# Optimization experiments

Measured on AMD Instinct MI355X. Metric: run time of the kernel, lower is better.

## Reference

```python
import jax, jax.numpy as jnp
import numpy as np

N = 50000      # nodes
D = 128        # in = hidden = out channels
L = 3          # num_layers
E = 320000     # edges per edge type
EPS_BN = 1e-5
EPS_NORM = 1e-12


def setup_inputs() -> dict:
    key = jax.random.key(0)
    ks = jax.random.split(key, 16)
    s = 1.0 / np.sqrt(D)
    inp = {}
    inp['x'] = jax.random.normal(ks[0], (N, D), jnp.float32)
    inp['edge_index0'] = jax.random.randint(ks[1], (2, E), 0, N, jnp.int32)
    inp['edge_index1'] = jax.random.randint(ks[2], (2, E), 0, N, jnp.int32)
    inp['W0'] = jax.random.normal(ks[3], (L, D, D), jnp.float32) * s
    inp['b0'] = jnp.zeros((L, D), jnp.float32)
    inp['W1'] = jax.random.normal(ks[4], (L, D, D), jnp.float32) * s
    inp['b1'] = jnp.zeros((L, D), jnp.float32)
    inp['gamma'] = jnp.ones((L, D), jnp.float32)
    inp['beta'] = jnp.zeros((L, D), jnp.float32)
    inp['emb1_W'] = jax.random.normal(ks[5], (D, D), jnp.float32) * s
    inp['emb1_b'] = jnp.zeros((D,), jnp.float32)
    inp['emb2_W'] = jax.random.normal(ks[6], (D, D), jnp.float32) * s
    inp['emb2_b'] = jnp.zeros((D,), jnp.float32)
    inp['ph1_Wa'] = jax.random.normal(ks[7], (D, D), jnp.float32) * s
    inp['ph1_ba'] = jnp.zeros((D,), jnp.float32)
    inp['ph1_Wb'] = jax.random.normal(ks[8], (D, D), jnp.float32) * s
    inp['ph1_bb'] = jnp.zeros((D,), jnp.float32)
    inp['ph2_Wa'] = jax.random.normal(ks[9], (D, D), jnp.float32) * s
    inp['ph2_ba'] = jnp.zeros((D,), jnp.float32)
    inp['ph2_Wb'] = jax.random.normal(ks[10], (D, D), jnp.float32) * s
    inp['ph2_bb'] = jnp.zeros((D,), jnp.float32)
    return inp


def _gcn(h_in, W, b, src, dst):
    # PyG GCNConv: add self-loops, symmetric deg^{-1/2} normalization, then scatter-add.
    h = h_in @ W                                   # [N, D]
    ones = jnp.ones(src.shape[0], h.dtype)
    deg = jax.ops.segment_sum(ones, dst, num_segments=N) + 1.0   # +1 self-loop
    dinv = jax.lax.rsqrt(deg)
    coef = (dinv[src] * dinv[dst])[:, None]        # [E, 1]
    agg = jax.ops.segment_sum(h[src] * coef, dst, num_segments=N)
    agg = agg + h * (dinv * dinv)[:, None]         # self-loop contribution
    return agg + b


def _bn(x, g, bt):
    # training-mode BatchNorm1d (batch statistics, biased variance)
    mu = jnp.mean(x, axis=0)
    var = jnp.mean(jnp.square(x - mu), axis=0)
    return (x - mu) * jax.lax.rsqrt(var + EPS_BN) * g + bt


def _l2norm(x):
    n = jnp.sqrt(jnp.sum(x * x, axis=1, keepdims=True))
    return x / jnp.maximum(n, EPS_NORM)


def reference(x, edge_index0, edge_index1, W0, b0, W1, b1, gamma, beta,
              emb1_W, emb1_b, emb2_W, emb2_b,
              ph1_Wa, ph1_ba, ph1_Wb, ph1_bb,
              ph2_Wa, ph2_ba, ph2_Wb, ph2_bb):
    s0, d0 = edge_index0[0], edge_index0[1]
    s1, d1 = edge_index1[0], edge_index1[1]
    h = x
    for i in range(L):
        # HeteroConv with aggr='sum': sum of the two edge-type GCNConv outputs
        h = _gcn(h, W0[i], b0[i], s0, d0) + _gcn(h, W1[i], b1[i], s1, d1)
        h = _bn(h, gamma[i], beta[i])
        if i < L - 1:
            h = jax.nn.relu(h)   # dropout omitted (deterministic / eval)
    e1 = jnp.tanh(h @ emb1_W + emb1_b)
    e2 = _l2norm(jnp.tanh(h @ emb2_W + emb2_b))
    p1 = _l2norm(jax.nn.relu(e1 @ ph1_Wa + ph1_ba) @ ph1_Wb + ph1_bb)
    p2 = _l2norm(jax.nn.relu(e2 @ ph2_Wa + ph2_ba) @ ph2_Wb + ph2_bb)
    return (e1, e2, p1, p2)
```

## Files before the change

### kernel.cpp

```cpp
#include <hip/hip_runtime.h>
#include <cstdint>
#include <cstddef>

#define D 128

typedef __attribute__((ext_vector_type(8))) short bf16x8;
typedef __attribute__((ext_vector_type(4))) float f32x4;
typedef __attribute__((ext_vector_type(8))) _Float16 f16x8;

__device__ __forceinline__ unsigned short f2bf(float f) {
  unsigned int u = __float_as_uint(f);
  unsigned int r = u + 0x7FFFu + ((u >> 16) & 1u);
  return (unsigned short)(r >> 16);
}
__device__ __forceinline__ float bf2f(unsigned short h) {
  return __uint_as_float((unsigned int)h << 16);
}
__device__ __forceinline__ float fast_tanh(float x) {
  float cx = fminf(fmaxf(x, -15.f), 15.f);
  float e = __expf(2.f * cx);
  return (e - 1.f) * __builtin_amdgcn_rcpf(e + 1.f);
}

struct WPtrs { const float* w[12]; };

__global__ __launch_bounds__(256) void packcount_kernel(
    WPtrs P, unsigned short* __restrict__ Wp,
    const int* __restrict__ d0, const int* __restrict__ d1,
    int* __restrict__ cnt, int E, int N, int packBlocks) {
  if ((int)blockIdx.x < packBlocks) {
    int tid = blockIdx.x * 256 + threadIdx.x;
    int m = tid >> 14;
    int r = tid & 16383;
    int b = r & 7, lane = (r >> 3) & 63, ks = (r >> 9) & 3, jt = r >> 11;
    int k = ks * 32 + ((lane >> 4) << 3) + b;
    int j = jt * 16 + (lane & 15);
    float w = P.w[m][k * 128 + j];
    unsigned short h = f2bf(w);
    Wp[m * 32768 + r] = h;
    Wp[m * 32768 + 16384 + r] = f2bf(w - bf2f(h));
  } else {
    int e = ((int)blockIdx.x - packBlocks) * 256 + threadIdx.x;
    if (e < E) {
      atomicAdd(&cnt[d0[e]], 1);
      atomicAdd(&cnt[N + d1[e]], 1);
    }
  }
}

__global__ __launch_bounds__(256) void scan_part_kernel(const int* __restrict__ cnt,
                                                        int* __restrict__ off,
                                                        int* __restrict__ bsum, int n2) {
  __shared__ int sh[256];
  int t = threadIdx.x;
  int i0 = blockIdx.x * 512 + 2 * t;
  int a0 = (i0 < n2) ? cnt[i0] : 0;
  int a1 = (i0 + 1 < n2) ? cnt[i0 + 1] : 0;
  int s = a0 + a1;
  sh[t] = s;
  __syncthreads();
  for (int d = 1; d < 256; d <<= 1) {
    int v = (t >= d) ? sh[t - d] : 0;
    __syncthreads();
    sh[t] += v;
    __syncthreads();
  }
  int p = sh[t] - s;
  if (i0 < n2) off[i0] = p;
  if (i0 + 1 < n2) off[i0 + 1] = p + a0;
  if (t == 255) bsum[blockIdx.x] = sh[255];
}

__global__ __launch_bounds__(256) void scan_bsum_kernel(int* __restrict__ bsum, int nb,
                                                        int* __restrict__ off_total) {
  __shared__ int sh[256];
  int t = threadIdx.x;
  int s = (t < nb) ? bsum[t] : 0;
  sh[t] = s;
  __syncthreads();
  for (int d = 1; d < 256; d <<= 1) {
    int v = (t >= d) ? sh[t - d] : 0;
    __syncthreads();
    sh[t] += v;
    __syncthreads();
  }
  if (t < nb) bsum[t] = sh[t] - s;
  if (t == 255) *off_total = sh[255];
}

__global__ __launch_bounds__(256) void scan_add_kernel(int* __restrict__ off,
                                                       const int* __restrict__ bsum,
                                                       int* __restrict__ cnt,
                                                       float* __restrict__ dinv, int n2) {
  int add = bsum[blockIdx.x];
  int base = blockIdx.x * 512;
#pragma unroll
  for (int u = 0; u < 2; u++) {
    int i = base + threadIdx.x + u * 256;
    if (i < n2) {
      off[i] += add;
      dinv[i] = rsqrtf((float)cnt[i] + 1.0f);
      cnt[i] = 0;
    }
  }
}

__global__ void fill_kernel(const int* __restrict__ ei0, const int* __restrict__ ei1,
                            const int* __restrict__ off, int* __restrict__ cnt,
                            int* __restrict__ csr, int E, int N) {
  int e = blockIdx.x * blockDim.x + threadIdx.x;
  if (e < E) {
    int s = ei0[e], d = ei0[E + e];
    int p = atomicAdd(&cnt[d], 1);
    csr[off[d] + p] = s;
    s = ei1[e]; d = ei1[E + e];
    p = atomicAdd(&cnt[N + d], 1);
    csr[off[N + d] + p] = s;
  }
}

__device__ __forceinline__ void split8(const float vv[8], bf16x8& hh, bf16x8& hl) {
#pragma unroll
  for (int c = 0; c < 8; c++) {
    unsigned short h = f2bf(vv[c]);
    hh[c] = (short)h;
    hl[c] = (short)f2bf(vv[c] - bf2f(h));
  }
}

template <int BN>
__global__ __launch_bounds__(256) void mm_dual(
    const unsigned short* __restrict__ Wp, const float* __restrict__ Af,
    const float* __restrict__ stats, const float* __restrict__ g0,
    const float* __restrict__ bt0, const float* __restrict__ dinv,
    _Float16* __restrict__ tab0, _Float16* __restrict__ tab1,
    int n, int N, float invn) {
  __shared__ float bnsc[128], bnsh[128];
  if (BN) {
    int t = threadIdx.x;
    if (t < 128) {
      float s = 0.f, q = 0.f;
#pragma unroll
      for (int r = 0; r < 8; r++) { s += stats[r * 128 + t]; q += stats[1024 + r * 128 + t]; }
      float mu = s * invn, var = q * invn - mu * mu;
      float sc = g0[t] * rsqrtf(var + 1e-5f);
      bnsc[t] = sc; bnsh[t] = bt0[t] - mu * sc;
    }
    __syncthreads();
  }
  constexpr int WJT = 4, WIT = 4;
  const int lane = threadIdx.x & 63;
  const int wid = threadIdx.x >> 6;
  const int wj = wid % 4, wi = wid / 4;
  const int jtbase = wj * WJT;
  const int ibase = blockIdx.x * 64 + wi * WIT * 16;
  const int lrow = lane & 15, lgrp = lane >> 4;

  int node[WIT];
  bool valid[WIT];
#pragma unroll
  for (int it = 0; it < WIT; it++) {
    int i = ibase + it * 16 + lrow;
    valid[it] = (i < n);
    node[it] = valid[it] ? i : (n - 1);
  }

  f32x4 acc[WJT][WIT];
#pragma unroll
  for (int jt = 0; jt < WJT; jt++)
#pragma unroll
    for (int it = 0; it < WIT; it++) acc[jt][it] = (f32x4){0.f, 0.f, 0.f, 0.f};

#pragma unroll
  for (int ks = 0; ks < 4; ks++) {
    float sck[8], shk[8];
    if (BN) {
      int cb = ks * 32 + lgrp * 8;
#pragma unroll
      for (int c = 0; c < 8; c++) { sck[c] = bnsc[cb + c]; shk[c] = bnsh[cb + c]; }
    }
    bf16x8 awh[WJT], awl[WJT];
#pragma unroll
    for (int jt = 0; jt < WJT; jt++) {
      int jg = jtbase + jt;
      const unsigned short* base = Wp + ((jg >= 8) ? 32768 : 0);
      size_t fo = (size_t)(((jg & 7) * 4 + ks) * 64 + lane) * 8;
      awh[jt] = *(const bf16x8*)(base + fo);
      awl[jt] = *(const bf16x8*)(base + fo + 16384);
    }
#pragma unroll
    for (int it = 0; it < WIT; it++) {
      const float* src = Af + (size_t)node[it] * 128 + ks * 32 + lgrp * 8;
      float4 u0 = *(const float4*)src;
      float4 u1 = *(const float4*)(src + 4);
      float vv[8] = {u0.x, u0.y, u0.z, u0.w, u1.x, u1.y, u1.z, u1.w};
      if (BN) {
#pragma unroll
        for (int c = 0; c < 8; c++) vv[c] = fmaxf(vv[c] * sck[c] + shk[c], 0.f);
      }
      bf16x8 bhh, bhl;
      split8(vv, bhh, bhl);
#pragma unroll
      for (int jt = 0; jt < WJT; jt++) {
        acc[jt][it] = __builtin_amdgcn_mfma_f32_16x16x32_bf16(awh[jt], bhh, acc[jt][it], 0, 0, 0);
        acc[jt][it] = __builtin_amdgcn_mfma_f32_16x16x32_bf16(awl[jt], bhh, acc[jt][it], 0, 0, 0);
        acc[jt][it] = __builtin_amdgcn_mfma_f32_16x16x32_bf16(awh[jt], bhl, acc[jt][it], 0, 0, 0);
      }
    }
  }

#pragma unroll
  for (int it = 0; it < WIT; it++) {
    if (!valid[it]) continue;
    float d0v = dinv[node[it]];
    float d1v = dinv[N + node[it]];
#pragma unroll
    for (int jt = 0; jt < WJT; jt++) {
      int jg = jtbase + jt;
      float s = (jg < 8) ? d0v : d1v;
      _Float16 o[4];
#pragma unroll
      for (int c = 0; c < 4; c++) o[c] = (_Float16)(acc[jt][it][c] * s);
      _Float16* base = (jg < 8)
          ? (tab0 + (size_t)node[it] * 128 + jg * 16)
          : (tab1 + (size_t)node[it] * 128 + (jg - 8) * 16);
      *(uint2*)(base + lgrp * 4) = *(uint2*)o;
    }
  }
}

__global__ __launch_bounds__(256) void gather_kernel(
    const _Float16* __restrict__ tab0, const _Float16* __restrict__ tab1,
    const float* __restrict__ dinv, const int* __restrict__ off,
    const int* __restrict__ csr,
    const float* __restrict__ b0, const float* __restrict__ b1,
    float* __restrict__ outh, float* __restrict__ stats, int n, int N) {
  __shared__ float reds[4][128];
  __shared__ float redq[4][128];
  int t = threadIdx.x;
  int g = t >> 4, l = t & 15;
  int node = blockIdx.x * 16 + g;
  bool valid = node < n;
  int nd = valid ? node : 0;
  const f16x8* t0 = (const f16x8*)tab0;
  const f16x8* t1 = (const f16x8*)tab1;
  float s0[8] = {0,0,0,0,0,0,0,0}, s1[8] = {0,0,0,0,0,0,0,0};
  if (valid) {
    f16x8 v = t0[(size_t)nd * 16 + l];
#pragma unroll
    for (int c = 0; c < 8; c++) s0[c] = (float)v[c];
    v = t1[(size_t)nd * 16 + l];
#pragma unroll
    for (int c = 0; c < 8; c++) s1[c] = (float)v[c];
  }
  int a = valid ? off[nd] : 0, b = valid ? off[nd + 1] : 0;
  int j = a;
  for (; j + 3 < b; j += 4) {
    int i0 = csr[j], i1 = csr[j + 1], i2 = csr[j + 2], i3 = csr[j + 3];
    f16x8 v0 = t0[(size_t)i0 * 16 + l];
    f16x8 v1 = t0[(size_t)i1 * 16 + l];
    f16x8 v2 = t0[(size_t)i2 * 16 + l];
    f16x8 v3 = t0[(size_t)i3 * 16 + l];
#pragma unroll
    for (int c = 0; c < 8; c++)
      s0[c] += ((float)v0[c] + (float)v1[c]) + ((float)v2[c] + (float)v3[c]);
  }
  for (; j < b; j++) {
    f16x8 va = t0[(size_t)csr[j] * 16 + l];
#pragma unroll
    for (int c = 0; c < 8; c++) s0[c] += (float)va[c];
  }
  a = valid ? off[N + nd] : 0; b = valid ? off[N + nd + 1] : 0;
  j = a;
  for (; j + 3 < b; j += 4) {
    int i0 = csr[j], i1 = csr[j + 1], i2 = csr[j + 2], i3 = csr[j + 3];
    f16x8 v0 = t1[(size_t)i0 * 16 + l];
    f16x8 v1 = t1[(size_t)i1 * 16 + l];
    f16x8 v2 = t1[(size_t)i2 * 16 + l];
    f16x8 v3 = t1[(size_t)i3 * 16 + l];
#pragma unroll
    for (int c = 0; c < 8; c++)
      s1[c] += ((float)v0[c] + (float)v1[c]) + ((float)v2[c] + (float)v3[c]);
  }
  for (; j < b; j++) {
    f16x8 va = t1[(size_t)csr[j] * 16 + l];
#pragma unroll
    for (int c = 0; c < 8; c++) s1[c] += (float)va[c];
  }
  float o[8] = {0,0,0,0,0,0,0,0};
  if (valid) {
    float d0 = dinv[nd], d1 = dinv[N + nd];
    const float4* B0 = (const float4*)(b0 + l * 8);
    const float4* B1 = (const float4*)(b1 + l * 8);
    float4 ba0 = B0[0], ba1 = B0[1], bb0 = B1[0], bb1 = B1[1];
    float bs[8] = {ba0.x + bb0.x, ba0.y + bb0.y, ba0.z + bb0.z, ba0.w + bb0.w,
                   ba1.x + bb1.x, ba1.y + bb1.y, ba1.z + bb1.z, ba1.w + bb1.w};
#pragma unroll
    for (int c = 0; c < 8; c++) o[c] = d0 * s0[c] + d1 * s1[c] + bs[c];
    float* dst = outh + (size_t)nd * 128 + l * 8;
    *(float4*)dst = make_float4(o[0], o[1], o[2], o[3]);
    *(float4*)(dst + 4) = make_float4(o[4], o[5], o[6], o[7]);
  }
  float sv[8], q[8];
#pragma unroll
  for (int c = 0; c < 8; c++) { sv[c] = o[c]; q[c] = o[c] * o[c]; }
#pragma unroll
  for (int c = 0; c < 8; c++) {
    sv[c] += __shfl_xor(sv[c], 16); sv[c] += __shfl_xor(sv[c], 32);
    q[c] += __shfl_xor(q[c], 16);  q[c] += __shfl_xor(q[c], 32);
  }
  int lane = t & 63, wid = t >> 6;
  if (lane < 16) {
#pragma unroll
    for (int c = 0; c < 8; c++) { reds[wid][lane * 8 + c] = sv[c]; redq[wid][lane * 8 + c] = q[c]; }
  }
  __syncthreads();
  if (t < 128) {
    float ts = reds[0][t] + reds[1][t] + reds[2][t] + reds[3][t];
    float tq = redq[0][t] + redq[1][t] + redq[2][t] + redq[3][t];
    int cp = blockIdx.x & 7;
    atomicAdd(&stats[cp * 128 + t], ts);
    atomicAdd(&stats[1024 + cp * 128 + t], tq);
  }
}

#define TP 132
__global__ __launch_bounds__(256) void heads3_kernel(
    const unsigned short* __restrict__ Wp,
    const float* __restrict__ h, const float* __restrict__ stats,
    const float* __restrict__ g2, const float* __restrict__ bt2,
    const float* __restrict__ emb1_b, const float* __restrict__ emb2_b,
    const float* __restrict__ ph1_ba, const float* __restrict__ ph1_bb,
    const float* __restrict__ ph2_ba, const float* __restrict__ ph2_bb,
    float* __restrict__ out, int n, float invn) {
  __shared__ float bnsc[128], bnsh[128];
  __shared__ float tile[2][64 * TP];
  __shared__ float l2red[2][4][16][2];
  const int t = threadIdx.x;
  if (t < 128) {
    float s = 0.f, q = 0.f;
#pragma unroll
    for (int r = 0; r < 8; r++) { s += stats[r * 128 + t]; q += stats[1024 + r * 128 + t]; }
    float mu = s * invn, var = q * invn - mu * mu;
    float sc = g2[t] * rsqrtf(var + 1e-5f);
    bnsc[t] = sc; bnsh[t] = bt2[t] - mu * sc;
  }
  __syncthreads();

  const int lane = t & 63, wid = t >> 6;
  const int wj = wid & 1, wh = wid >> 1;
  const int lrow = lane & 15, lgrp = lane >> 4;
  const int jtbase = wj * 4;
  const int base = blockIdx.x * 64;
  const size_t ND = (size_t)n * 128;
  float* myt = &tile[wh][0];

  int node[4];
  bool valid[4];
#pragma unroll
  for (int it = 0; it < 4; it++) {
    int i = base + it * 16 + lrow;
    valid[it] = (i < n);
    node[it] = valid[it] ? i : (n - 1);
  }

  f32x4 acc[4][4];
  const unsigned short* slot;
  const float* bias;

  slot = Wp + (size_t)(6 + wh) * 32768;
  bias = wh ? emb2_b : emb1_b;
#pragma unroll
  for (int jt = 0; jt < 4; jt++) {
    float4 b4 = *(const float4*)(bias + (jtbase + jt) * 16 + lgrp * 4);
#pragma unroll
    for (int it = 0; it < 4; it++) acc[jt][it] = (f32x4){b4.x, b4.y, b4.z, b4.w};
  }
#pragma unroll
  for (int ks = 0; ks < 4; ks++) {
    int cb = ks * 32 + lgrp * 8;
    float sck[8], shk[8];
#pragma unroll
    for (int c = 0; c < 8; c++) { sck[c] = bnsc[cb + c]; shk[c] = bnsh[cb + c]; }
    bf16x8 awh[4], awl[4];
#pragma unroll
    for (int jt = 0; jt < 4; jt++) {
      size_t fo = (size_t)(((jtbase + jt) * 4 + ks) * 64 + lane) * 8;
      awh[jt] = *(const bf16x8*)(slot + fo);
      awl[jt] = *(const bf16x8*)(slot + fo + 16384);
    }
#pragma unroll
    for (int it = 0; it < 4; it++) {
      const float* src = h + (size_t)node[it] * 128 + cb;
      float4 u0 = *(const float4*)src;
      float4 u1 = *(const float4*)(src + 4);
      float vv[8] = {u0.x, u0.y, u0.z, u0.w, u1.x, u1.y, u1.z, u1.w};
#pragma unroll
      for (int c = 0; c < 8; c++) vv[c] = vv[c] * sck[c] + shk[c];
      bf16x8 bhh, bhl;
      split8(vv, bhh, bhl);
#pragma unroll
      for (int jt = 0; jt < 4; jt++) {
        acc[jt][it] = __builtin_amdgcn_mfma_f32_16x16x32_bf16(awh[jt], bhh, acc[jt][it], 0, 0, 0);
        acc[jt][it] = __builtin_amdgcn_mfma_f32_16x16x32_bf16(awl[jt], bhh, acc[jt][it], 0, 0, 0);
        acc[jt][it] = __builtin_amdgcn_mfma_f32_16x16x32_bf16(awh[jt], bhl, acc[jt][it], 0, 0, 0);
      }
    }
  }
#pragma unroll
  for (int jt = 0; jt < 4; jt++)
#pragma unroll
    for (int it = 0; it < 4; it++)
#pragma unroll
      for (int c = 0; c < 4; c++) acc[jt][it][c] = fast_tanh(acc[jt][it][c]);

  float rsv[4];
  if (wh == 1) {
#pragma unroll
    for (int it = 0; it < 4; it++) {
      float rs = 0.f;
#pragma unroll
      for (int jt = 0; jt < 4; jt++)
#pragma unroll
        for (int c = 0; c < 4; c++) rs += acc[jt][it][c] * acc[jt][it][c];
      rs += __shfl_xor(rs, 16);
      rs += __shfl_xor(rs, 32);
      rsv[it] = rs;
      if (lane < 16) l2red[1][it][lane][wj] = rs;
    }
  }
  __syncthreads();
  if (wh == 1) {
#pragma unroll
    for (int it = 0; it < 4; it++) {
      float full = rsv[it] + l2red[1][it][lrow][wj ^ 1];
      float scl = 1.f / fmaxf(sqrtf(full), 1e-12f);
#pragma unroll
      for (int jt = 0; jt < 4; jt++)
#pragma unroll
        for (int c = 0; c < 4; c++) acc[jt][it][c] *= scl;
    }
  }
#pragma unroll
  for (int it = 0; it < 4; it++) {
#pragma unroll
    for (int jt = 0; jt < 4; jt++) {
      float4 v = make_float4(acc[jt][it][0], acc[jt][it][1], acc[jt][it][2], acc[jt][it][3]);
      *(float4*)(myt + (it * 16 + lrow) * TP + (jtbase + jt) * 16 + lgrp * 4) = v;
      if (valid[it])
        *(float4*)(out + (size_t)wh * ND + (size_t)node[it] * 128 + (jtbase + jt) * 16 + lgrp * 4) = v;
    }
  }
  __syncthreads();

  slot = Wp + (size_t)(8 + 2 * wh) * 32768;
  bias = wh ? ph2_ba : ph1_ba;
#pragma unroll
  for (int jt = 0; jt < 4; jt++) {
    float4 b4 = *(const float4*)(bias + (jtbase + jt) * 16 + lgrp * 4);
#pragma unroll
    for (int it = 0; it < 4; it++) acc[jt][it] = (f32x4){b4.x, b4.y, b4.z, b4.w};
  }
#pragma unroll
  for (int ks = 0; ks < 4; ks++) {
    bf16x8 awh[4], awl[4];
#pragma unroll
    for (int jt = 0; jt < 4; jt++) {
      size_t fo = (size_t)(((jtbase + jt) * 4 + ks) * 64 + lane) * 8;
      awh[jt] = *(const bf16x8*)(slot + fo);
      awl[jt] = *(const bf16x8*)(slot + fo + 16384);
    }
#pragma unroll
    for (int it = 0; it < 4; it++) {
      const float* src = myt + (it * 16 + lrow) * TP + ks * 32 + lgrp * 8;
      float4 u0 = *(const float4*)src;
      float4 u1 = *(const float4*)(src + 4);
      float vv[8] = {u0.x, u0.y, u0.z, u0.w, u1.x, u1.y, u1.z, u1.w};
      bf16x8 bhh, bhl;
      split8(vv, bhh, bhl);
#pragma unroll
      for (int jt = 0; jt < 4; jt++) {
        acc[jt][it] = __builtin_amdgcn_mfma_f32_16x16x32_bf16(awh[jt], bhh, acc[jt][it], 0, 0, 0);
        acc[jt][it] = __builtin_amdgcn_mfma_f32_16x16x32_bf16(awl[jt], bhh, acc[jt][it], 0, 0, 0);
        acc[jt][it] = __builtin_amdgcn_mfma_f32_16x16x32_bf16(awh[jt], bhl, acc[jt][it], 0, 0, 0);
      }
    }
  }
#pragma unroll
  for (int jt = 0; jt < 4; jt++)
#pragma unroll
    for (int it = 0; it < 4; it++)
#pragma unroll
      for (int c = 0; c < 4; c++) acc[jt][it][c] = fmaxf(acc[jt][it][c], 0.f);
  __syncthreads();
#pragma unroll
  for (int it = 0; it < 4; it++)
#pragma unroll
    for (int jt = 0; jt < 4; jt++)
      *(float4*)(myt + (it * 16 + lrow) * TP + (jtbase + jt) * 16 + lgrp * 4) =
          make_float4(acc[jt][it][0], acc[jt][it][1], acc[jt][it][2], acc[jt][it][3]);
  __syncthreads();

  slot = Wp + (size_t)(9 + 2 * wh) * 32768;
  bias = wh ? ph2_bb : ph1_bb;
#pragma unroll
  for (int jt = 0; jt < 4; jt++) {
    float4 b4 = *(const float4*)(bias + (jtbase + jt) * 16 + lgrp * 4);
#pragma unroll
    for (int it = 0; it < 4; it++) acc[jt][it] = (f32x4){b4.x, b4.y, b4.z, b4.w};
  }
#pragma unroll
  for (int ks = 0; ks < 4; ks++) {
    bf16x8 awh[4], awl[4];
#pragma unroll
    for (int jt = 0; jt < 4; jt++) {
      size_t fo = (size_t)(((jtbase + jt) * 4 + ks) * 64 + lane) * 8;
      awh[jt] = *(const bf16x8*)(slot + fo);
      awl[jt] = *(const bf16x8*)(slot + fo + 16384);
    }
#pragma unroll
    for (int it = 0; it < 4; it++) {
      const float* src = myt + (it * 16 + lrow) * TP + ks * 32 + lgrp * 8;
      float4 u0 = *(const float4*)src;
      float4 u1 = *(const float4*)(src + 4);
      float vv[8] = {u0.x, u0.y, u0.z, u0.w, u1.x, u1.y, u1.z, u1.w};
      bf16x8 bhh, bhl;
      split8(vv, bhh, bhl);
#pragma unroll
      for (int jt = 0; jt < 4; jt++) {
        acc[jt][it] = __builtin_amdgcn_mfma_f32_16x16x32_bf16(awh[jt], bhh, acc[jt][it], 0, 0, 0);
        acc[jt][it] = __builtin_amdgcn_mfma_f32_16x16x32_bf16(awl[jt], bhh, acc[jt][it], 0, 0, 0);
        acc[jt][it] = __builtin_amdgcn_mfma_f32_16x16x32_bf16(awh[jt], bhl, acc[jt][it], 0, 0, 0);
      }
    }
  }
#pragma unroll
  for (int it = 0; it < 4; it++) {
    float rs = 0.f;
#pragma unroll
    for (int jt = 0; jt < 4; jt++)
#pragma unroll
      for (int c = 0; c < 4; c++) rs += acc[jt][it][c] * acc[jt][it][c];
    rs += __shfl_xor(rs, 16);
    rs += __shfl_xor(rs, 32);
    rsv[it] = rs;
    if (lane < 16) l2red[wh][it][lane][wj] = rs;
  }
  __syncthreads();
#pragma unroll
  for (int it = 0; it < 4; it++) {
    float full = rsv[it] + l2red[wh][it][lrow][wj ^ 1];
    float scl = 1.f / fmaxf(sqrtf(full), 1e-12f);
    if (!valid[it]) continue;
#pragma unroll
    for (int jt = 0; jt < 4; jt++)
      *(float4*)(out + (size_t)(2 + wh) * ND + (size_t)node[it] * 128 + (jtbase + jt) * 16 + lgrp * 4) =
          make_float4(acc[jt][it][0] * scl, acc[jt][it][1] * scl,
                      acc[jt][it][2] * scl, acc[jt][it][3] * scl);
  }
}

extern "C" void kernel_launch(void* const* d_in, const int* in_sizes, int n_in,
                              void* d_out, int out_size, void* d_ws, size_t ws_size,
                              hipStream_t stream) {
  const float* x      = (const float*)d_in[0];
  const int*   ei0    = (const int*)d_in[1];
  const int*   ei1    = (const int*)d_in[2];
  const float* W0     = (const float*)d_in[3];
  const float* b0     = (const float*)d_in[4];
  const float* W1     = (const float*)d_in[5];
  const float* b1     = (const float*)d_in[6];
  const float* gamma  = (const float*)d_in[7];
  const float* beta   = (const float*)d_in[8];
  const float* emb1_W = (const float*)d_in[9];
  const float* emb1_b = (const float*)d_in[10];
  const float* emb2_W = (const float*)d_in[11];
  const float* emb2_b = (const float*)d_in[12];
  const float* ph1_Wa = (const float*)d_in[13];
  const float* ph1_ba = (const float*)d_in[14];
  const float* ph1_Wb = (const float*)d_in[15];
  const float* ph1_bb = (const float*)d_in[16];
  const float* ph2_Wa = (const float*)d_in[17];
  const float* ph2_ba = (const float*)d_in[18];
  const float* ph2_Wb = (const float*)d_in[19];
  const float* ph2_bb = (const float*)d_in[20];

  const int N = in_sizes[0] / D;
  const int E = in_sizes[1] / 2;
  const int N2 = 2 * N;
  const size_t ND = (size_t)N * D;
  const float invn = 1.0f / (float)N;
  float* out = (float*)d_out;

  char* p = (char*)d_ws;
  auto carve = [&](size_t bytes) -> void* {
    void* r = (void*)p;
    p += (bytes + 255) & ~(size_t)255;
    return r;
  };
  int*   cnt   = (int*)carve((size_t)N2 * 4);
  float* stats = (float*)carve((size_t)3 * 2048 * 4);
  size_t zbytes = (size_t)((char*)(stats + 3 * 2048) - (char*)cnt);
  int*   off   = (int*)carve((size_t)(N2 + 1) * 4);
  float* dinv  = (float*)carve((size_t)N2 * 4);
  int*   csr   = (int*)carve((size_t)2 * E * 4);
  int*   bsum  = (int*)carve(256 * 4);
  unsigned short* Wp = (unsigned short*)carve((size_t)12 * 32768 * 2);
  float* hbuf = (float*)carve(4 * ND);
  _Float16* tab0 = (_Float16*)carve(2 * ND);
  _Float16* tab1 = (_Float16*)carve(2 * ND);

  const int TPB = 256;
  const int packBlocks = 768;
  const int gridPC = packBlocks + (E + TPB - 1) / TPB;
  const int gridE = (E + TPB - 1) / TPB;
  const int nbScan = (N2 + 511) / 512;
  const int gridDual = (N + 63) / 64;
  const int gridGath = (N + 15) / 16;
  const int gridH3 = (N + 63) / 64;

  WPtrs P;
  P.w[0] = W0;                     P.w[1] = W1;
  P.w[2] = W0 + (size_t)D * D;     P.w[3] = W1 + (size_t)D * D;
  P.w[4] = W0 + (size_t)2 * D * D; P.w[5] = W1 + (size_t)2 * D * D;
  P.w[6] = emb1_W; P.w[7] = emb2_W;
  P.w[8] = ph1_Wa; P.w[9] = ph1_Wb;
  P.w[10] = ph2_Wa; P.w[11] = ph2_Wb;

  hipMemsetAsync(cnt, 0, zbytes, stream);
  packcount_kernel<<<gridPC, TPB, 0, stream>>>(P, Wp, ei0 + E, ei1 + E, cnt, E, N, packBlocks);
  scan_part_kernel<<<nbScan, TPB, 0, stream>>>(cnt, off, bsum, N2);
  scan_bsum_kernel<<<1, TPB, 0, stream>>>(bsum, nbScan, off + N2);
  scan_add_kernel<<<nbScan, TPB, 0, stream>>>(off, bsum, cnt, dinv, N2);
  fill_kernel<<<gridE, TPB, 0, stream>>>(ei0, ei1, off, cnt, csr, E, N);

  for (int i = 0; i < 3; i++) {
    const unsigned short* wslot = Wp + (size_t)(2 * i) * 32768;
    if (i == 0) {
      mm_dual<0><<<gridDual, TPB, 0, stream>>>(wslot, x, nullptr, nullptr, nullptr,
                                               dinv, tab0, tab1, N, N, invn);
    } else {
      mm_dual<1><<<gridDual, TPB, 0, stream>>>(wslot, hbuf, stats + (size_t)(i - 1) * 2048,
                                               gamma + (i - 1) * D, beta + (i - 1) * D,
                                               dinv, tab0, tab1, N, N, invn);
    }
    gather_kernel<<<gridGath, TPB, 0, stream>>>(tab0, tab1, dinv, off, csr,
                                                b0 + i * D, b1 + i * D, hbuf,
                                                stats + (size_t)i * 2048, N, N);
  }

  heads3_kernel<<<gridH3, TPB, 0, stream>>>(
      Wp, hbuf, stats + (size_t)2 * 2048, gamma + 2 * D, beta + 2 * D,
      emb1_b, emb2_b, ph1_ba, ph1_bb, ph2_ba, ph2_bb, out, N, invn);
}
```

Measured before the change: 348.4 us.

## Fuse CSR fill with first-layer matmul and use fp16 split in head MLPs

Merges the CSR fill kernel and the layer-0 dual matmul into one launch, with separate block ranges doing each job. This removes a launch and lets the two independent workloads run side by side. The second-stage head matmuls now stage activations in shared memory as fp16 and use fp16 MFMAs with a hi/lo split of the weights only, dropping the activation low part. That cuts MFMA count by a third, removes the split8 conversions and halves LDS use, at the cost of fp16 precision on the activations.

```diff
diff --git a/kernel.cpp b/kernel.cpp
--- a/kernel.cpp
+++ b/kernel.cpp
@@ -21,6 +21,7 @@
   float e = __expf(2.f * cx);
   return (e - 1.f) * __builtin_amdgcn_rcpf(e + 1.f);
 }
+union HU { _Float16 f; unsigned short u; };
 
 struct WPtrs { const float* w[12]; };
 
@@ -36,9 +37,17 @@
     int k = ks * 32 + ((lane >> 4) << 3) + b;
     int j = jt * 16 + (lane & 15);
     float w = P.w[m][k * 128 + j];
-    unsigned short h = f2bf(w);
-    Wp[m * 32768 + r] = h;
-    Wp[m * 32768 + 16384 + r] = f2bf(w - bf2f(h));
+    if (m < 8) {
+      unsigned short h = f2bf(w);
+      Wp[m * 32768 + r] = h;
+      Wp[m * 32768 + 16384 + r] = f2bf(w - bf2f(h));
+    } else {
+      HU hh, ll;
+      hh.f = (_Float16)w;
+      ll.f = (_Float16)(w - (float)hh.f);
+      Wp[m * 32768 + r] = hh.u;
+      Wp[m * 32768 + 16384 + r] = ll.u;
+    }
   } else {
     int e = ((int)blockIdx.x - packBlocks) * 256 + threadIdx.x;
     if (e < E) {
@@ -105,20 +114,6 @@
   }
 }
 
-__global__ void fill_kernel(const int* __restrict__ ei0, const int* __restrict__ ei1,
-                            const int* __restrict__ off, int* __restrict__ cnt,
-                            int* __restrict__ csr, int E, int N) {
-  int e = blockIdx.x * blockDim.x + threadIdx.x;
-  if (e < E) {
-    int s = ei0[e], d = ei0[E + e];
-    int p = atomicAdd(&cnt[d], 1);
-    csr[off[d] + p] = s;
-    s = ei1[e]; d = ei1[E + e];
-    p = atomicAdd(&cnt[N + d], 1);
-    csr[off[N + d] + p] = s;
-  }
-}
-
 __device__ __forceinline__ void split8(const float vv[8], bf16x8& hh, bf16x8& hl) {
 #pragma unroll
   for (int c = 0; c < 8; c++) {
@@ -129,8 +124,8 @@
 }
 
 template <int BN>
-__global__ __launch_bounds__(256) void mm_dual(
-    const unsigned short* __restrict__ Wp, const float* __restrict__ Af,
+__device__ __forceinline__ void mm_dual_body(
+    int bid, const unsigned short* __restrict__ Wp, const float* __restrict__ Af,
     const float* __restrict__ stats, const float* __restrict__ g0,
     const float* __restrict__ bt0, const float* __restrict__ dinv,
     _Float16* __restrict__ tab0, _Float16* __restrict__ tab1,
@@ -153,7 +148,7 @@
   const int wid = threadIdx.x >> 6;
   const int wj = wid % 4, wi = wid / 4;
   const int jtbase = wj * WJT;
-  const int ibase = blockIdx.x * 64 + wi * WIT * 16;
+  const int ibase = bid * 64 + wi * WIT * 16;
   const int lrow = lane & 15, lgrp = lane >> 4;
 
   int node[WIT];
@@ -226,6 +221,38 @@
           : (tab1 + (size_t)node[it] * 128 + (jg - 8) * 16);
       *(uint2*)(base + lgrp * 4) = *(uint2*)o;
     }
+  }
+}
+
+__global__ __launch_bounds__(256) void mm_dual_k(
+    const unsigned short* __restrict__ Wp, const float* __restrict__ Af,
+    const float* __restrict__ stats, const float* __restrict__ g0,
+    const float* __restrict__ bt0, const float* __restrict__ dinv,
+    _Float16* __restrict__ tab0, _Float16* __restrict__ tab1,
+    int n, int N, float invn) {
+  mm_dual_body<1>(blockIdx.x, Wp, Af, stats, g0, bt0, dinv, tab0, tab1, n, N, invn);
+}
+
+__global__ __launch_bounds__(256) void fillmm0_kernel(
+    const int* __restrict__ ei0, const int* __restrict__ ei1,
+    const int* __restrict__ off, int* __restrict__ cnt, int* __restrict__ csr,
+    int E, int fillBlocks,
+    const unsigned short* __restrict__ Wp, const float* __restrict__ x,
+    const float* __restrict__ dinv, _Float16* __restrict__ tab0,
+    _Float16* __restrict__ tab1, int n, int N) {
+  if ((int)blockIdx.x < fillBlocks) {
+    int e = blockIdx.x * 256 + threadIdx.x;
+    if (e < E) {
+      int s = ei0[e], d = ei0[E + e];
+      int p = atomicAdd(&cnt[d], 1);
+      csr[off[d] + p] = s;
+      s = ei1[e]; d = ei1[E + e];
+      p = atomicAdd(&cnt[N + d], 1);
+      csr[off[N + d] + p] = s;
+    }
+  } else {
+    mm_dual_body<0>(blockIdx.x - fillBlocks, Wp, x, nullptr, nullptr, nullptr,
+                    dinv, tab0, tab1, n, N, 0.f);
   }
 }
 
@@ -324,7 +351,7 @@
   }
 }
 
-#define TP 132
+#define TPH 136
 __global__ __launch_bounds__(256) void heads3_kernel(
     const unsigned short* __restrict__ Wp,
     const float* __restrict__ h, const float* __restrict__ stats,
@@ -334,7 +361,7 @@
     const float* __restrict__ ph2_ba, const float* __restrict__ ph2_bb,
     float* __restrict__ out, int n, float invn) {
   __shared__ float bnsc[128], bnsh[128];
-  __shared__ float tile[2][64 * TP];
+  __shared__ _Float16 tile[2][64 * TPH];
   __shared__ float l2red[2][4][16][2];
   const int t = threadIdx.x;
   if (t < 128) {
@@ -353,7 +380,7 @@
   const int jtbase = wj * 4;
   const int base = blockIdx.x * 64;
   const size_t ND = (size_t)n * 128;
-  float* myt = &tile[wh][0];
+  _Float16* myt = &tile[wh][0];
 
   int node[4];
   bool valid[4];
@@ -445,10 +472,13 @@
   for (int it = 0; it < 4; it++) {
 #pragma unroll
     for (int jt = 0; jt < 4; jt++) {
-      float4 v = make_float4(acc[jt][it][0], acc[jt][it][1], acc[jt][it][2], acc[jt][it][3]);
-      *(float4*)(myt + (it * 16 + lrow) * TP + (jtbase + jt) * 16 + lgrp * 4) = v;
       if (valid[it])
-        *(float4*)(out + (size_t)wh * ND + (size_t)node[it] * 128 + (jtbase + jt) * 16 + lgrp * 4) = v;
+        *(float4*)(out + (size_t)wh * ND + (size_t)node[it] * 128 + (jtbase + jt) * 16 + lgrp * 4) =
+            make_float4(acc[jt][it][0], acc[jt][it][1], acc[jt][it][2], acc[jt][it][3]);
+      _Float16 o4[4];
+#pragma unroll
+      for (int c = 0; c < 4; c++) o4[c] = (_Float16)acc[jt][it][c];
+      *(uint2*)(myt + (it * 16 + lrow) * TPH + (jtbase + jt) * 16 + lgrp * 4) = *(uint2*)o4;
     }
   }
   __syncthreads();
@@ -463,26 +493,20 @@
   }
 #pragma unroll
   for (int ks = 0; ks < 4; ks++) {
-    bf16x8 awh[4], awl[4];
+    f16x8 awh[4], awl[4];
 #pragma unroll
     for (int jt = 0; jt < 4; jt++) {
       size_t fo = (size_t)(((jtbase + jt) * 4 + ks) * 64 + lane) * 8;
-      awh[jt] = *(const bf16x8*)(slot + fo);
-      awl[jt] = *(const bf16x8*)(slot + fo + 16384);
+      awh[jt] = *(const f16x8*)(slot + fo);
+      awl[jt] = *(const f16x8*)(slot + fo + 16384);
     }
 #pragma unroll
     for (int it = 0; it < 4; it++) {
-      const float* src = myt + (it * 16 + lrow) * TP + ks * 32 + lgrp * 8;
-      float4 u0 = *(const float4*)src;
-      float4 u1 = *(const float4*)(src + 4);
-      float vv[8] = {u0.x, u0.y, u0.z, u0.w, u1.x, u1.y, u1.z, u1.w};
-      bf16x8 bhh, bhl;
-      split8(vv, bhh, bhl);
+      f16x8 bh = *(const f16x8*)(myt + (it * 16 + lrow) * TPH + ks * 32 + lgrp * 8);
 #pragma unroll
       for (int jt = 0; jt < 4; jt++) {
-        acc[jt][it] = __builtin_amdgcn_mfma_f32_16x16x32_bf16(awh[jt], bhh, acc[jt][it], 0, 0, 0);
-        acc[jt][it] = __builtin_amdgcn_mfma_f32_16x16x32_bf16(awl[jt], bhh, acc[jt][it], 0, 0, 0);
-        acc[jt][it] = __builtin_amdgcn_mfma_f32_16x16x32_bf16(awh[jt], bhl, acc[jt][it], 0, 0, 0);
+        acc[jt][it] = __builtin_amdgcn_mfma_f32_16x16x32_f16(awh[jt], bh, acc[jt][it], 0, 0, 0);
+        acc[jt][it] = __builtin_amdgcn_mfma_f32_16x16x32_f16(awl[jt], bh, acc[jt][it], 0, 0, 0);
       }
     }
   }
@@ -496,9 +520,12 @@
 #pragma unroll
   for (int it = 0; it < 4; it++)
 #pragma unroll
-    for (int jt = 0; jt < 4; jt++)
-      *(float4*)(myt + (it * 16 + lrow) * TP + (jtbase + jt) * 16 + lgrp * 4) =
-          make_float4(acc[jt][it][0], acc[jt][it][1], acc[jt][it][2], acc[jt][it][3]);
+    for (int jt = 0; jt < 4; jt++) {
+      _Float16 o4[4];
+#pragma unroll
+      for (int c = 0; c < 4; c++) o4[c] = (_Float16)acc[jt][it][c];
+      *(uint2*)(myt + (it * 16 + lrow) * TPH + (jtbase + jt) * 16 + lgrp * 4) = *(uint2*)o4;
+    }
   __syncthreads();
 
   slot = Wp + (size_t)(9 + 2 * wh) * 32768;
@@ -511,26 +538,20 @@
   }
 #pragma unroll
   for (int ks = 0; ks < 4; ks++) {
-    bf16x8 awh[4], awl[4];
+    f16x8 awh[4], awl[4];
 #pragma unroll
     for (int jt = 0; jt < 4; jt++) {
       size_t fo = (size_t)(((jtbase + jt) * 4 + ks) * 64 + lane) * 8;
-      awh[jt] = *(const bf16x8*)(slot + fo);
-      awl[jt] = *(const bf16x8*)(slot + fo + 16384);
+      awh[jt] = *(const f16x8*)(slot + fo);
+      awl[jt] = *(const f16x8*)(slot + fo + 16384);
     }
 #pragma unroll
     for (int it = 0; it < 4; it++) {
-      const float* src = myt + (it * 16 + lrow) * TP + ks * 32 + lgrp * 8;
-      float4 u0 = *(const float4*)src;
-      float4 u1 = *(const float4*)(src + 4);
-      float vv[8] = {u0.x, u0.y, u0.z, u0.w, u1.x, u1.y, u1.z, u1.w};
-      bf16x8 bhh, bhl;
-      split8(vv, bhh, bhl);
+      f16x8 bh = *(const f16x8*)(myt + (it * 16 + lrow) * TPH + ks * 32 + lgrp * 8);
 #pragma unroll
       for (int jt = 0; jt < 4; jt++) {
-        acc[jt][it] = __builtin_amdgcn_mfma_f32_16x16x32_bf16(awh[jt], bhh, acc[jt][it], 0, 0, 0);
-        acc[jt][it] = __builtin_amdgcn_mfma_f32_16x16x32_bf16(awl[jt], bhh, acc[jt][it], 0, 0, 0);
-        acc[jt][it] = __builtin_amdgcn_mfma_f32_16x16x32_bf16(awh[jt], bhl, acc[jt][it], 0, 0, 0);
+        acc[jt][it] = __builtin_amdgcn_mfma_f32_16x16x32_f16(awh[jt], bh, acc[jt][it], 0, 0, 0);
+        acc[jt][it] = __builtin_amdgcn_mfma_f32_16x16x32_f16(awl[jt], bh, acc[jt][it], 0, 0, 0);
       }
     }
   }
@@ -613,7 +634,7 @@
   const int TPB = 256;
   const int packBlocks = 768;
   const int gridPC = packBlocks + (E + TPB - 1) / TPB;
-  const int gridE = (E + TPB - 1) / TPB;
+  const int fillBlocks = (E + TPB - 1) / TPB;
   const int nbScan = (N2 + 511) / 512;
   const int gridDual = (N + 63) / 64;
   const int gridGath = (N + 15) / 16;
@@ -632,18 +653,16 @@
   scan_part_kernel<<<nbScan, TPB, 0, stream>>>(cnt, off, bsum, N2);
   scan_bsum_kernel<<<1, TPB, 0, stream>>>(bsum, nbScan, off + N2);
   scan_add_kernel<<<nbScan, TPB, 0, stream>>>(off, bsum, cnt, dinv, N2);
-  fill_kernel<<<gridE, TPB, 0, stream>>>(ei0, ei1, off, cnt, csr, E, N);
-
-  for (int i = 0; i < 3; i++) {
-    const unsigned short* wslot = Wp + (size_t)(2 * i) * 32768;
-    if (i == 0) {
-      mm_dual<0><<<gridDual, TPB, 0, stream>>>(wslot, x, nullptr, nullptr, nullptr,
-                                               dinv, tab0, tab1, N, N, invn);
-    } else {
-      mm_dual<1><<<gridDual, TPB, 0, stream>>>(wslot, hbuf, stats + (size_t)(i - 1) * 2048,
-                                               gamma + (i - 1) * D, beta + (i - 1) * D,
-                                               dinv, tab0, tab1, N, N, invn);
-    }
+
+  fillmm0_kernel<<<fillBlocks + gridDual, TPB, 0, stream>>>(
+      ei0, ei1, off, cnt, csr, E, fillBlocks, Wp, x, dinv, tab0, tab1, N, N);
+  gather_kernel<<<gridGath, TPB, 0, stream>>>(tab0, tab1, dinv, off, csr,
+                                              b0, b1, hbuf, stats, N, N);
+  for (int i = 1; i < 3; i++) {
+    mm_dual_k<<<gridDual, TPB, 0, stream>>>(Wp + (size_t)(2 * i) * 32768, hbuf,
+                                            stats + (size_t)(i - 1) * 2048,
+                                            gamma + (i - 1) * D, beta + (i - 1) * D,
+                                            dinv, tab0, tab1, N, N, invn);
     gather_kernel<<<gridGath, TPB, 0, stream>>>(tab0, tab1, dinv, off, csr,
                                                 b0 + i * D, b1 + i * D, hbuf,
                                                 stats + (size_t)i * 2048, N, N);
```

Result: faster. 329.1 us (-5.6%).
